# Performance work log

Measured on AMD Instinct MI355X. Metric: run time of the kernel, lower is better.

The kernel has to match this reference:

```python
import jax, jax.numpy as jnp
import numpy as np

H_IMG, W_IMG = 2160, 3840


def _avgpool3x3(x):
    # AvgPool2d(3, stride=1, padding=1), count_include_pad=True -> divide by 9 always
    s = jax.lax.reduce_window(x, 0.0, jax.lax.add, (3, 3, 1), (1, 1, 1), 'SAME')
    return s / 9.0


def setup_inputs() -> dict:
    key = jax.random.key(0)
    k1, k2, k3, k4 = jax.random.split(key, 4)
    depth = jax.random.uniform(k1, (H_IMG, W_IMG), jnp.float32) * 4.0 + 0.5
    rgb = jax.random.uniform(k2, (H_IMG, W_IMG, 3), jnp.float32)
    mask = jax.random.randint(k3, (H_IMG, W_IMG), 0, 2, jnp.int32)
    l = jax.random.normal(k4, (9, 3), jnp.float32) * 0.3
    fx = fy = 3000.0
    cx, cy = W_IMG / 2.0, H_IMG / 2.0
    CameraParam = jnp.array([[fx, 0.0, cx], [0.0, fy, cy], [0.0, 0.0, 1.0]], jnp.float32)
    return {'depth': depth, 'rgb': rgb, 'mask': mask, 'l': l, 'CameraParam': CameraParam}


def reference(depth, rgb, mask, l, CameraParam):
    nrows, ncols = depth.shape
    imask = mask > 0                      # [H, W] bool
    m3 = imask[..., None]                 # [H, W, 1]

    # Homogeneous pixel grid -> back-projected rays (precomputed in torch __init__)
    yy, xx = jnp.meshgrid(jnp.arange(nrows, dtype=jnp.float32),
                          jnp.arange(ncols, dtype=jnp.float32), indexing='ij')
    p2d = jnp.stack([xx, yy, jnp.ones_like(xx)], axis=-1)      # [H, W, 3]
    Kinv = jnp.linalg.inv(CameraParam)
    p3d = jnp.einsum('ij,hwj->hwi', Kinv, p2d)                 # [H, W, 3]

    # Depth -> 3D points, shifted neighbors (zero-padded at borders)
    p = p3d * depth[..., None]                                 # [H, W, 3]
    pl = jnp.pad(p[:, 1:, :], ((0, 0), (0, 1), (0, 0)))        # right neighbor
    pu = jnp.pad(p[1:, :, :], ((0, 1), (0, 0), (0, 0)))        # down neighbor

    n = jnp.cross(pl - p, pu - p)                              # [H, W, 3]
    norm = jnp.linalg.norm(n, axis=-1, keepdims=True)
    n = n / jnp.maximum(norm, 1e-12)                           # F.normalize

    nx, ny, nz = n[..., 0], n[..., 1], n[..., 2]
    ones = jnp.ones_like(nx)
    Hsh = jnp.stack([ones, ny, nz, nx, nx * ny, ny * nz,
                     -nx * nx - ny * ny + 2.0 * nz * nz,
                     nz * nx, nx * nx - ny * ny], axis=-1)     # [H, W, 9]
    B = jnp.einsum('hwk,kc->hwc', Hsh, l)                      # [H, W, 3]

    # Scatter into full image: zero outside mask (matches render_img[imask] = B)
    render = jnp.where(m3, B, 0.0)
    render_mean = jax.lax.stop_gradient(_avgpool3x3(render))   # render_img.detach()
    rgbmean = _avgpool3x3(jax.lax.stop_gradient(rgb))          # rgb.detach()

    diff = (render - render_mean) - (rgb - rgbmean)
    cnt = jnp.sum(imask).astype(jnp.float32) * 3.0             # MSE over masked elems
    loss = jnp.sum(jnp.where(m3, diff * diff, 0.0)) / cnt
    return loss
```

## Files before the change

### kernel.cpp

```cpp
#include <hip/hip_runtime.h>
#include <math.h>

#define H_IMG 2160
#define W_IMG 3840
#define SPAN 120
#define NSX 32
#define HS 10
#define WPB 4
#define NSY 54
#define NBLOCKS (NSX * NSY)
#define NBINS 2048

__global__ __launch_bounds__(256, 4) void shading_main(
    const float* __restrict__ depth,
    const float* __restrict__ rgb,
    const int*   __restrict__ mask,
    const float* __restrict__ lmat,
    const float* __restrict__ K,
    float* __restrict__ accum,
    int direct)
{
    const int tid  = threadIdx.x;
    const int lane = tid & 63;
    const int wv   = tid >> 6;
    const int sx   = blockIdx.x;
    const int x0   = sx * SPAN;
    const int y0   = blockIdx.y * (WPB * HS) + wv * HS;
    const int colBase  = x0 + 2 * lane;
    const int colBase3 = 3 * colBase;
    const bool fullIn = (colBase + 1) < W_IMG;

    const float m00 = K[0], m01 = K[1], m02 = K[2];
    const float m10 = K[3], m11 = K[4], m12 = K[5];
    const float m20 = K[6], m21 = K[7], m22 = K[8];
    const float det = m00*(m11*m22 - m12*m21)
                    - m01*(m10*m22 - m12*m20)
                    + m02*(m10*m21 - m11*m20);
    const float id  = 1.0f / det;
    const float i00 = (m11*m22 - m12*m21) * id;
    const float i01 = (m02*m21 - m01*m22) * id;
    const float i02 = (m01*m12 - m02*m11) * id;
    const float i10 = (m12*m20 - m10*m22) * id;
    const float i11 = (m00*m22 - m02*m20) * id;
    const float i12 = (m02*m10 - m00*m12) * id;
    const float i20 = (m10*m21 - m11*m20) * id;
    const float i21 = (m01*m20 - m00*m21) * id;
    const float i22 = (m00*m11 - m01*m10) * id;

    float L[27];
    #pragma unroll
    for (int i = 0; i < 27; ++i) L[i] = lmat[i];

    float wout[2];
    #pragma unroll
    for (int k = 0; k < 2; ++k) {
        const int c  = colBase + k;
        const int lc = 2 * lane + k;
        const bool v = (c < W_IMG) && (lc <= SPAN) && (lc >= 1 || sx == 0);
        wout[k] = v ? 1.0f : 0.0f;
    }
    const float qm1s = (lane == 0) ? 0.0f : 1.0f;

    float rx = fmaf(i00, (float)colBase, fmaf(i01, (float)(y0 - 1), i02));
    float ry = fmaf(i10, (float)colBase, fmaf(i11, (float)(y0 - 1), i12));
    float rz = fmaf(i20, (float)colBase, fmaf(i21, (float)(y0 - 1), i22));

    const float2 Z2 = make_float2(0.f, 0.f);

    float2 d0 = Z2, d1 = Z2, d2 = Z2;
    float2 raE = Z2, rbE = Z2, rcE = Z2;  int2 mE = make_int2(0, 0);
    float2 raO = Z2, rbO = Z2, rcO = Z2;  int2 mO = make_int2(0, 0);

    if (fullIn) {
        if (y0 > 0) {
            const size_t r = (size_t)(y0 - 1);
            d0  = *(const float2*)(depth + r * W_IMG + colBase);
            raE = *(const float2*)(rgb + r * (3 * W_IMG) + colBase3);
            rbE = *(const float2*)(rgb + r * (3 * W_IMG) + colBase3 + 2);
            rcE = *(const float2*)(rgb + r * (3 * W_IMG) + colBase3 + 4);
            mE  = *(const int2*)(mask + r * W_IMG + colBase);
        }
        {
            const size_t r = (size_t)y0;
            d1  = *(const float2*)(depth + r * W_IMG + colBase);
            raO = *(const float2*)(rgb + r * (3 * W_IMG) + colBase3);
            rbO = *(const float2*)(rgb + r * (3 * W_IMG) + colBase3 + 2);
            rcO = *(const float2*)(rgb + r * (3 * W_IMG) + colBase3 + 4);
            mO  = *(const int2*)(mask + r * W_IMG + colBase);
        }
        d2 = *(const float2*)(depth + (size_t)(y0 + 1) * W_IMG + colBase);
    }

    float sA0[2] = {0,0}, sA1[2] = {0,0}, sA2[2] = {0,0};
    float sB0[2] = {0,0}, sB1[2] = {0,0}, sB2[2] = {0,0};
    float qB0[2] = {0,0}, qB1[2] = {0,0}, qB2[2] = {0,0};
    float wB[2]  = {0,0};
    float accS = 0.f, accC = 0.f;

#define BODY(DC, DN, RA, RB, RC, MM, HD, HR, EM) do {                          \
    const float dc0 = DC.x, dc1 = DC.y;                                        \
    const float dn0 = DN.x, dn1 = DN.y;                                        \
    const float rr0 = RA.x, rr1 = RA.y, rr2 = RB.x;                            \
    const float rr3 = RB.y, rr4 = RC.x, rr5 = RC.y;                            \
    const int   mm0 = MM.x, mm1 = MM.y;                                        \
    const float dcR = __shfl_down(DC.x, 1, 64);                                \
                                  \
    {                                                                          \
        const int hD = (HD);                                                   \
        DC = Z2;                                                               \
        if (fullIn && hD < H_IMG)                                              \
            DC = *(const float2*)(depth + (size_t)hD * W_IMG + colBase);       \
        const int hR = (HR);                                                   \
        RA = Z2; RB = Z2; RC = Z2; MM = make_int2(0, 0);                       \
        if (fullIn && hR < H_IMG) {                                            \
            const float* rr = rgb + (size_t)hR * (3 * W_IMG);                  \
            RA = *(const float2*)(rr + colBase3);                              \
            RB = *(const float2*)(rr + colBase3 + 2);                          \
            RC = *(const float2*)(rr + colBase3 + 4);                          \
            MM = *(const int2*)(mask + (size_t)hR * W_IMG + colBase);          \
        }                                                                      \
    }                                                                          \
    float qC0[2], qC1[2], qC2[2], wC[2];                                       \
    {                                                                          \
        const float dcv[2] = {dc0, dc1};                                       \
        const float dnv[2] = {dn0, dn1};                                       \
        const float rrv[6] = {rr0, rr1, rr2, rr3, rr4, rr5};                   \
        const int   mmv[2] = {mm0, mm1};                                       \
        float rxk = rx, ryk = ry, rzk = rz;                                    \
        _Pragma("unroll")                                                      \
        for (int k = 0; k < 2; ++k) {                                          \
            const float dd0 = dcv[k];                                          \
            const float dR = (k == 0) ? dcv[1] : dcR;                          \
            const float dD = dnv[k];                                           \
            const float px = rxk * dd0, py = ryk * dd0, pz = rzk * dd0;        \
            const float ax = (rxk + i00) * dR - px;                            \
            const float ay = (ryk + i10) * dR - py;                            \
            const float az = (rzk + i20) * dR - pz;                            \
            const float bx = (rxk + i01) * dD - px;                            \
            const float by = (ryk + i11) * dD - py;                            \
            const float bz = (rzk + i21) * dD - pz;                            \
            float nx = ay*bz - az*by;                                          \
            float ny = az*bx - ax*bz;                                          \
            float nz = ax*by - ay*bx;                                          \
            const float nn  = nx*nx + ny*ny + nz*nz;                           \
            const float inr = __builtin_amdgcn_rsqf(fmaxf(nn, 1e-24f));        \
            nx *= inr; ny *= inr; nz *= inr;                                   \
            const float h4 = nx*ny, h5 = ny*nz, h7 = nz*nx;                    \
            const float nx2 = nx*nx, ny2 = ny*ny, nz2 = nz*nz;                 \
            const float h6 = 2.f*nz2 - nx2 - ny2;                              \
            const float h8 = nx2 - ny2;                                        \
            const float B0 = L[0] + ny*L[3] + nz*L[6] + nx*L[9]  + h4*L[12]    \
                           + h5*L[15] + h6*L[18] + h7*L[21] + h8*L[24];        \
            const float B1 = L[1] + ny*L[4] + nz*L[7] + nx*L[10] + h4*L[13]    \
                           + h5*L[16] + h6*L[19] + h7*L[22] + h8*L[25];        \
            const float B2 = L[2] + ny*L[5] + nz*L[8] + nx*L[11] + h4*L[14]    \
                           + h5*L[17] + h6*L[20] + h7*L[23] + h8*L[26];        \
            const float m  = (mmv[k] > 0) ? 1.0f : 0.0f;                       \
            qC0[k] = fmaf(m, B0, -rrv[3*k + 0]);                               \
            qC1[k] = fmaf(m, B1, -rrv[3*k + 1]);                               \
            qC2[k] = fmaf(m, B2, -rrv[3*k + 2]);                               \
            wC[k]  = m * wout[k];                                              \
            rxk += i00; ryk += i10; rzk += i20;                                \
        }                                                                      \
    }                                                                          \
                           \
    float sC0[2], sC1[2], sC2[2];                                              \
    {                                                                          \
        const float a0 = __shfl_up(qC0[1], 1, 64) * qm1s;                      \
        const float a1 = __shfl_up(qC1[1], 1, 64) * qm1s;                      \
        const float a2 = __shfl_up(qC2[1], 1, 64) * qm1s;                      \
        const float p0 = __shfl_down(qC0[0], 1, 64);                           \
        const float p1 = __shfl_down(qC1[0], 1, 64);                           \
        const float p2 = __shfl_down(qC2[0], 1, 64);                           \
        const float t0 = qC0[0] + qC0[1];                                      \
        sC0[0] = a0 + t0;  sC0[1] = t0 + p0;                                   \
        const float t1 = qC1[0] + qC1[1];                                      \
        sC1[0] = a1 + t1;  sC1[1] = t1 + p1;                                   \
        const float t2 = qC2[0] + qC2[1];                                      \
        sC2[0] = a2 + t2;  sC2[1] = t2 + p2;                                   \
    }                                                                          \
                                        \
    if (EM) {                                                                  \
        _Pragma("unroll")                                                      \
        for (int k = 0; k < 2; ++k) {                                          \
            const float v0 = sA0[k] + sB0[k] + sC0[k];                         \
            const float v1 = sA1[k] + sB1[k] + sC1[k];                         \
            const float v2 = sA2[k] + sB2[k] + sC2[k];                         \
            const float e0 = fmaf(v0, -(1.f/9.f), qB0[k]);                     \
            const float e1 = fmaf(v1, -(1.f/9.f), qB1[k]);                     \
            const float e2 = fmaf(v2, -(1.f/9.f), qB2[k]);                     \
            const float w  = wB[k];                                            \
            accS = fmaf(w, e0*e0 + e1*e1 + e2*e2, accS);                       \
            accC += w;                                                         \
        }                                                                      \
    }                                                                          \
    _Pragma("unroll")                                                          \
    for (int k = 0; k < 2; ++k) {                                              \
        sA0[k] = sB0[k]; sA1[k] = sB1[k]; sA2[k] = sB2[k];                     \
        sB0[k] = sC0[k]; sB1[k] = sC1[k]; sB2[k] = sC2[k];                     \
        qB0[k] = qC0[k]; qB1[k] = qC1[k]; qB2[k] = qC2[k];                     \
        wB[k]  = wC[k];                                                        \
    }                                                                          \
    rx += i01; ry += i11; rz += i21;                                           \
} while (0)

    int hb = y0 - 1;
    #pragma unroll 1
    for (int t = 0; t < (HS + 2) / 6; ++t) {
        const bool em = (t >= 1);
        BODY(d0, d1, raE, rbE, rcE, mE, hb + 3, hb + 2, em);
        BODY(d1, d2, raO, rbO, rcO, mO, hb + 4, hb + 3, em);
        BODY(d2, d0, raE, rbE, rcE, mE, hb + 5, hb + 4, true);
        BODY(d0, d1, raO, rbO, rcO, mO, hb + 6, hb + 5, true);
        BODY(d1, d2, raE, rbE, rcE, mE, hb + 7, hb + 6, true);
        BODY(d2, d0, raO, rbO, rcO, mO, hb + 8, hb + 7, true);
        hb += 6;
    }
#undef BODY

    #pragma unroll
    for (int off = 32; off > 0; off >>= 1) {
        accS += __shfl_down(accS, off, 64);
        accC += __shfl_down(accC, off, 64);
    }
    __shared__ float sS[WPB], sC[WPB];
    if (lane == 0) { sS[wv] = accS; sC[wv] = accC; }
    __syncthreads();
    if (tid == 0) {
        const float ts = sS[0] + sS[1] + sS[2] + sS[3];
        const float tc = sC[0] + sC[1] + sC[2] + sC[3];
        const int bid = blockIdx.y * gridDim.x + blockIdx.x;
        if (direct) {
            accum[2*bid + 0] = ts;
            accum[2*bid + 1] = tc;
        } else {
            const int bin = bid & (NBINS - 1);
            atomicAdd(&accum[2*bin + 0], ts);
            atomicAdd(&accum[2*bin + 1], tc);
        }
    }
}

__global__ __launch_bounds__(256) void finalize_kernel(
    const float* __restrict__ part, int n, float* __restrict__ out)
{
    const int tid = threadIdx.x;
    float s = 0.f, c = 0.f;
    for (int i = tid; i < n; i += 256) {
        s += part[2*i + 0];
        c += part[2*i + 1];
    }
    #pragma unroll
    for (int off = 32; off > 0; off >>= 1) {
        s += __shfl_down(s, off, 64);
        c += __shfl_down(c, off, 64);
    }
    __shared__ float sS[4], sC[4];
    const int wid = tid >> 6, lane = tid & 63;
    if (lane == 0) { sS[wid] = s; sC[wid] = c; }
    __syncthreads();
    if (tid == 0) {
        const float ts = sS[0] + sS[1] + sS[2] + sS[3];
        const float tc = sC[0] + sC[1] + sC[2] + sC[3];
        out[0] = ts / (3.0f * tc);
    }
}

extern "C" void kernel_launch(void* const* d_in, const int* in_sizes, int n_in,
                              void* d_out, int out_size, void* d_ws, size_t ws_size,
                              hipStream_t stream) {
    const float* depth = (const float*)d_in[0];
    const float* rgb   = (const float*)d_in[1];
    const int*   mask  = (const int*)  d_in[2];
    const float* lmat  = (const float*)d_in[3];
    const float* K     = (const float*)d_in[4];
    float* accum = (float*)d_ws;
    float* out   = (float*)d_out;

    const dim3 grid(NSX, NSY);

    if (ws_size >= (size_t)NBLOCKS * 2 * sizeof(float)) {
        shading_main<<<grid, 256, 0, stream>>>(depth, rgb, mask, lmat, K, accum, 1);
        finalize_kernel<<<1, 256, 0, stream>>>(accum, NBLOCKS, out);
    } else {
        hipMemsetAsync(accum, 0, NBINS * 2 * sizeof(float), stream);
        shading_main<<<grid, 256, 0, stream>>>(depth, rgb, mask, lmat, K, accum, 0);
        finalize_kernel<<<1, 256, 0, stream>>>(accum, NBINS, out);
    }
}
```

Measured before the change: 248.7 us.

## Shrink row strips, clamp last column tile, add unguarded interior loop

Reduces rows per wave from 10 to 8 and raises the grid height to keep the image covered. Clamps the last column tile so every lane reads in bounds, which removes the fullIn guard. Replaces the 6-way unrolled rotating-register body with a rolled loop using pointer increments, and adds a separate unguarded loop for interior strips. The changes aim to cut bounds-check overhead and spread work over more blocks, at the cost of more halo rows recomputed per strip and less unrolling to hide load latency.

```diff
diff --git a/kernel.cpp b/kernel.cpp
--- a/kernel.cpp
+++ b/kernel.cpp
@@ -5,9 +5,9 @@
 #define W_IMG 3840
 #define SPAN 120
 #define NSX 32
-#define HS 10
+#define HS 8
 #define WPB 4
-#define NSY 54
+#define NSY 68
 #define NBLOCKS (NSX * NSY)
 #define NBINS 2048
 
@@ -24,11 +24,10 @@
     const int lane = tid & 63;
     const int wv   = tid >> 6;
     const int sx   = blockIdx.x;
-    const int x0   = sx * SPAN;
+    const int x0   = min(sx * SPAN, W_IMG - 128);
     const int y0   = blockIdx.y * (WPB * HS) + wv * HS;
     const int colBase  = x0 + 2 * lane;
     const int colBase3 = 3 * colBase;
-    const bool fullIn = (colBase + 1) < W_IMG;
 
     const float m00 = K[0], m01 = K[1], m02 = K[2];
     const float m10 = K[3], m11 = K[4], m12 = K[5];
@@ -54,9 +53,9 @@
     float wout[2];
     #pragma unroll
     for (int k = 0; k < 2; ++k) {
-        const int c  = colBase + k;
-        const int lc = 2 * lane + k;
-        const bool v = (c < W_IMG) && (lc <= SPAN) && (lc >= 1 || sx == 0);
+        const int c   = colBase + k;
+        const int rel = c - sx * SPAN;
+        const bool v  = (c < W_IMG) && (rel <= SPAN) && (rel >= 1 || sx == 0);
         wout[k] = v ? 1.0f : 0.0f;
     }
     const float qm1s = (lane == 0) ? 0.0f : 1.0f;
@@ -67,29 +66,23 @@
 
     const float2 Z2 = make_float2(0.f, 0.f);
 
-    float2 d0 = Z2, d1 = Z2, d2 = Z2;
-    float2 raE = Z2, rbE = Z2, rcE = Z2;  int2 mE = make_int2(0, 0);
-    float2 raO = Z2, rbO = Z2, rcO = Z2;  int2 mO = make_int2(0, 0);
-
-    if (fullIn) {
-        if (y0 > 0) {
-            const size_t r = (size_t)(y0 - 1);
-            d0  = *(const float2*)(depth + r * W_IMG + colBase);
-            raE = *(const float2*)(rgb + r * (3 * W_IMG) + colBase3);
-            rbE = *(const float2*)(rgb + r * (3 * W_IMG) + colBase3 + 2);
-            rcE = *(const float2*)(rgb + r * (3 * W_IMG) + colBase3 + 4);
-            mE  = *(const int2*)(mask + r * W_IMG + colBase);
-        }
-        {
-            const size_t r = (size_t)y0;
-            d1  = *(const float2*)(depth + r * W_IMG + colBase);
-            raO = *(const float2*)(rgb + r * (3 * W_IMG) + colBase3);
-            rbO = *(const float2*)(rgb + r * (3 * W_IMG) + colBase3 + 2);
-            rcO = *(const float2*)(rgb + r * (3 * W_IMG) + colBase3 + 4);
-            mO  = *(const int2*)(mask + r * W_IMG + colBase);
-        }
-        d2 = *(const float2*)(depth + (size_t)(y0 + 1) * W_IMG + colBase);
-    }
+    float2 dC = Z2, dN = Z2;
+    float2 raC = Z2, rbC = Z2, rcC = Z2;
+    int2   mC  = make_int2(0, 0);
+    if (y0 > 0 && (y0 - 1) < H_IMG) {
+        const size_t r = (size_t)(y0 - 1);
+        dC  = *(const float2*)(depth + r * W_IMG + colBase);
+        raC = *(const float2*)(rgb + r * (3 * W_IMG) + colBase3);
+        rbC = *(const float2*)(rgb + r * (3 * W_IMG) + colBase3 + 2);
+        rcC = *(const float2*)(rgb + r * (3 * W_IMG) + colBase3 + 4);
+        mC  = *(const int2*)(mask + r * W_IMG + colBase);
+    }
+    if (y0 < H_IMG)
+        dN = *(const float2*)(depth + (size_t)y0 * W_IMG + colBase);
+
+    const float* pfD = depth + (size_t)(y0 + 1) * W_IMG + colBase;
+    const float* pfR = rgb   + (size_t)y0 * (3 * W_IMG) + colBase3;
+    const int*   pfM = mask  + (size_t)y0 * W_IMG + colBase;
 
     float sA0[2] = {0,0}, sA1[2] = {0,0}, sA2[2] = {0,0};
     float sB0[2] = {0,0}, sB1[2] = {0,0}, sB2[2] = {0,0};
@@ -97,42 +90,42 @@
     float wB[2]  = {0,0};
     float accS = 0.f, accC = 0.f;
 
-#define BODY(DC, DN, RA, RB, RC, MM, HD, HR, EM) do {                          \
-    const float dc0 = DC.x, dc1 = DC.y;                                        \
-    const float dn0 = DN.x, dn1 = DN.y;                                        \
-    const float rr0 = RA.x, rr1 = RA.y, rr2 = RB.x;                            \
-    const float rr3 = RB.y, rr4 = RC.x, rr5 = RC.y;                            \
-    const int   mm0 = MM.x, mm1 = MM.y;                                        \
-    const float dcR = __shfl_down(DC.x, 1, 64);                                \
-                                  \
-    {                                                                          \
-        const int hD = (HD);                                                   \
-        DC = Z2;                                                               \
-        if (fullIn && hD < H_IMG)                                              \
-            DC = *(const float2*)(depth + (size_t)hD * W_IMG + colBase);       \
-        const int hR = (HR);                                                   \
-        RA = Z2; RB = Z2; RC = Z2; MM = make_int2(0, 0);                       \
-        if (fullIn && hR < H_IMG) {                                            \
-            const float* rr = rgb + (size_t)hR * (3 * W_IMG);                  \
-            RA = *(const float2*)(rr + colBase3);                              \
-            RB = *(const float2*)(rr + colBase3 + 2);                          \
-            RC = *(const float2*)(rr + colBase3 + 4);                          \
-            MM = *(const int2*)(mask + (size_t)hR * W_IMG + colBase);          \
-        }                                                                      \
-    }                                                                          \
-    float qC0[2], qC1[2], qC2[2], wC[2];                                       \
-    {                                                                          \
-        const float dcv[2] = {dc0, dc1};                                       \
-        const float dnv[2] = {dn0, dn1};                                       \
-        const float rrv[6] = {rr0, rr1, rr2, rr3, rr4, rr5};                   \
-        const int   mmv[2] = {mm0, mm1};                                       \
+#define MAINLOOP(GUARD)                                                        \
+    _Pragma("unroll 1")                                                        \
+    for (int j = 0; j < HS + 2; ++j) {                                         \
+        float2 dP, raN, rbN, rcN; int2 mN;                                     \
+        if (GUARD) {                                                           \
+            dP = Z2; raN = Z2; rbN = Z2; rcN = Z2; mN = make_int2(0, 0);       \
+            if (y0 + 1 + j < H_IMG) dP = *(const float2*)pfD;                  \
+            if (y0 + j < H_IMG) {                                              \
+                raN = *(const float2*)(pfR);                                   \
+                rbN = *(const float2*)(pfR + 2);                               \
+                rcN = *(const float2*)(pfR + 4);                               \
+                mN  = *(const int2*)(pfM);                                     \
+            }                                                                  \
+        } else {                                                               \
+            dP  = *(const float2*)pfD;                                         \
+            raN = *(const float2*)(pfR);                                       \
+            rbN = *(const float2*)(pfR + 2);                                   \
+            rcN = *(const float2*)(pfR + 4);                                   \
+            mN  = *(const int2*)(pfM);                                         \
+        }                                                                      \
+        pfD += W_IMG; pfR += 3 * W_IMG; pfM += W_IMG;                          \
+                                                                               \
+        const float dcv[2] = {dC.x, dC.y};                                     \
+        const float dnv[2] = {dN.x, dN.y};                                     \
+        const float rrv[6] = {raC.x, raC.y, rbC.x, rbC.y, rcC.x, rcC.y};       \
+        const int   mmv[2] = {mC.x, mC.y};                                     \
+        const float dcR = __shfl_down(dC.x, 1, 64);                            \
+                                                                               \
+        float qC0[2], qC1[2], qC2[2], wC[2];                                   \
         float rxk = rx, ryk = ry, rzk = rz;                                    \
         _Pragma("unroll")                                                      \
         for (int k = 0; k < 2; ++k) {                                          \
-            const float dd0 = dcv[k];                                          \
+            const float d0 = dcv[k];                                           \
             const float dR = (k == 0) ? dcv[1] : dcR;                          \
             const float dD = dnv[k];                                           \
-            const float px = rxk * dd0, py = ryk * dd0, pz = rzk * dd0;        \
+            const float px = rxk * d0, py = ryk * d0, pz = rzk * d0;           \
             const float ax = (rxk + i00) * dR - px;                            \
             const float ay = (ryk + i10) * dR - py;                            \
             const float az = (rzk + i20) * dR - pz;                            \
@@ -162,61 +155,57 @@
             wC[k]  = m * wout[k];                                              \
             rxk += i00; ryk += i10; rzk += i20;                                \
         }                                                                      \
-    }                                                                          \
-                           \
-    float sC0[2], sC1[2], sC2[2];                                              \
-    {                                                                          \
-        const float a0 = __shfl_up(qC0[1], 1, 64) * qm1s;                      \
-        const float a1 = __shfl_up(qC1[1], 1, 64) * qm1s;                      \
-        const float a2 = __shfl_up(qC2[1], 1, 64) * qm1s;                      \
-        const float p0 = __shfl_down(qC0[0], 1, 64);                           \
-        const float p1 = __shfl_down(qC1[0], 1, 64);                           \
-        const float p2 = __shfl_down(qC2[0], 1, 64);                           \
-        const float t0 = qC0[0] + qC0[1];                                      \
-        sC0[0] = a0 + t0;  sC0[1] = t0 + p0;                                   \
-        const float t1 = qC1[0] + qC1[1];                                      \
-        sC1[0] = a1 + t1;  sC1[1] = t1 + p1;                                   \
-        const float t2 = qC2[0] + qC2[1];                                      \
-        sC2[0] = a2 + t2;  sC2[1] = t2 + p2;                                   \
-    }                                                                          \
-                                        \
-    if (EM) {                                                                  \
+                                                                               \
+        float sC0[2], sC1[2], sC2[2];                                          \
+        {                                                                      \
+            const float a0 = __shfl_up(qC0[1], 1, 64) * qm1s;                  \
+            const float a1 = __shfl_up(qC1[1], 1, 64) * qm1s;                  \
+            const float a2 = __shfl_up(qC2[1], 1, 64) * qm1s;                  \
+            const float p0 = __shfl_down(qC0[0], 1, 64);                       \
+            const float p1 = __shfl_down(qC1[0], 1, 64);                       \
+            const float p2 = __shfl_down(qC2[0], 1, 64);                       \
+            const float t0 = qC0[0] + qC0[1];                                  \
+            sC0[0] = a0 + t0;  sC0[1] = t0 + p0;                               \
+            const float t1 = qC1[0] + qC1[1];                                  \
+            sC1[0] = a1 + t1;  sC1[1] = t1 + p1;                               \
+            const float t2 = qC2[0] + qC2[1];                                  \
+            sC2[0] = a2 + t2;  sC2[1] = t2 + p2;                               \
+        }                                                                      \
+                                                                               \
+        if (j >= 2) {                                                          \
+            _Pragma("unroll")                                                  \
+            for (int k = 0; k < 2; ++k) {                                      \
+                const float v0 = sA0[k] + sB0[k] + sC0[k];                     \
+                const float v1 = sA1[k] + sB1[k] + sC1[k];                     \
+                const float v2 = sA2[k] + sB2[k] + sC2[k];                     \
+                const float e0 = fmaf(v0, -(1.f/9.f), qB0[k]);                 \
+                const float e1 = fmaf(v1, -(1.f/9.f), qB1[k]);                 \
+                const float e2 = fmaf(v2, -(1.f/9.f), qB2[k]);                 \
+                const float w  = wB[k];                                        \
+                accS = fmaf(w, e0*e0 + e1*e1 + e2*e2, accS);                   \
+                accC += w;                                                     \
+            }                                                                  \
+        }                                                                      \
+                                                                               \
         _Pragma("unroll")                                                      \
         for (int k = 0; k < 2; ++k) {                                          \
-            const float v0 = sA0[k] + sB0[k] + sC0[k];                         \
-            const float v1 = sA1[k] + sB1[k] + sC1[k];                         \
-            const float v2 = sA2[k] + sB2[k] + sC2[k];                         \
-            const float e0 = fmaf(v0, -(1.f/9.f), qB0[k]);                     \
-            const float e1 = fmaf(v1, -(1.f/9.f), qB1[k]);                     \
-            const float e2 = fmaf(v2, -(1.f/9.f), qB2[k]);                     \
-            const float w  = wB[k];                                            \
-            accS = fmaf(w, e0*e0 + e1*e1 + e2*e2, accS);                       \
-            accC += w;                                                         \
-        }                                                                      \
-    }                                                                          \
-    _Pragma("unroll")                                                          \
-    for (int k = 0; k < 2; ++k) {                                              \
-        sA0[k] = sB0[k]; sA1[k] = sB1[k]; sA2[k] = sB2[k];                     \
-        sB0[k] = sC0[k]; sB1[k] = sC1[k]; sB2[k] = sC2[k];                     \
-        qB0[k] = qC0[k]; qB1[k] = qC1[k]; qB2[k] = qC2[k];                     \
-        wB[k]  = wC[k];                                                        \
-    }                                                                          \
-    rx += i01; ry += i11; rz += i21;                                           \
-} while (0)
-
-    int hb = y0 - 1;
-    #pragma unroll 1
-    for (int t = 0; t < (HS + 2) / 6; ++t) {
-        const bool em = (t >= 1);
-        BODY(d0, d1, raE, rbE, rcE, mE, hb + 3, hb + 2, em);
-        BODY(d1, d2, raO, rbO, rcO, mO, hb + 4, hb + 3, em);
-        BODY(d2, d0, raE, rbE, rcE, mE, hb + 5, hb + 4, true);
-        BODY(d0, d1, raO, rbO, rcO, mO, hb + 6, hb + 5, true);
-        BODY(d1, d2, raE, rbE, rcE, mE, hb + 7, hb + 6, true);
-        BODY(d2, d0, raO, rbO, rcO, mO, hb + 8, hb + 7, true);
-        hb += 6;
-    }
-#undef BODY
+            sA0[k] = sB0[k]; sA1[k] = sB1[k]; sA2[k] = sB2[k];                 \
+            sB0[k] = sC0[k]; sB1[k] = sC1[k]; sB2[k] = sC2[k];                 \
+            qB0[k] = qC0[k]; qB1[k] = qC1[k]; qB2[k] = qC2[k];                 \
+            wB[k]  = wC[k];                                                    \
+        }                                                                      \
+        dC = dN; dN = dP;                                                      \
+        raC = raN; rbC = rbN; rcC = rcN; mC = mN;                              \
+        rx += i01; ry += i11; rz += i21;                                       \
+    }
+
+    const bool edge = (y0 == 0) || (y0 + HS + 2 > H_IMG - 1);
+    if (edge) {
+        MAINLOOP(1)
+    } else {
+        MAINLOOP(0)
+    }
+#undef MAINLOOP
 
     #pragma unroll
     for (int off = 32; off > 0; off >>= 1) {
```

After: 209.8 us. -15.6%, faster.
